# Performance work log

Hardware: AMD Instinct MI355X
Metric: run time of the kernel (lower is better)

Reference implementation:

```python
import jax, jax.numpy as jnp
import numpy as np

HIDDEN = 1024
NUM_HEADS = 16
HEAD_DIM = 64
B, S = 2, 2048


def setup_inputs() -> dict:
    key = jax.random.key(0)
    k1, k2, k3 = jax.random.split(key, 3)
    x = jax.random.normal(k1, (B, S, HIDDEN), dtype=jnp.float32)
    # xavier-uniform style scaling for the projection weights
    lim_qkv = (6.0 / (HIDDEN + 3 * NUM_HEADS * HEAD_DIM)) ** 0.5
    lim_o = (6.0 / (NUM_HEADS * HEAD_DIM + HIDDEN)) ** 0.5
    w_qkv = jax.random.uniform(k2, (HIDDEN, 3 * NUM_HEADS * HEAD_DIM), jnp.float32, -lim_qkv, lim_qkv)
    w_o = jax.random.uniform(k3, (NUM_HEADS * HEAD_DIM, HIDDEN), jnp.float32, -lim_o, lim_o)
    return {"x": x, "w_qkv": w_qkv, "w_o": w_o}


def reference(x, w_qkv, w_o):
    b, s, _ = x.shape
    qkv = jnp.einsum('bsh,hf->bsf', x, w_qkv)               # [b, s, 3*H*D]
    qkv = qkv.reshape(b, s, 3, NUM_HEADS, HEAD_DIM)
    q = jnp.transpose(qkv[:, :, 0], (0, 2, 1, 3))           # [b, h, s, d]
    k = jnp.transpose(qkv[:, :, 1], (0, 2, 3, 1))           # [b, h, d, s]
    v = jnp.transpose(qkv[:, :, 2], (0, 2, 1, 3))           # [b, h, s, d]
    scores = jnp.einsum('bhqd,bhdk->bhqk', q, k) / jnp.sqrt(jnp.float32(HEAD_DIM))
    scores = jax.nn.softmax(scores, axis=-1)                # [b, h, q, k]
    # NOTE: faithful to source bug: sums over q, output indexed by k
    values = jnp.einsum('bhqk,bhkd->bhkd', scores, v)       # [b, h, s, d]
    values = jnp.transpose(values, (0, 2, 1, 3)).reshape(b, s, NUM_HEADS * HEAD_DIM)
    return jnp.einsum('bsf,fh->bsh', values, w_o)
```

## Files before the change

### kernel.cpp

```cpp
#include <hip/hip_runtime.h>
#include <stdint.h>


#define DEV static __device__ __forceinline__

typedef unsigned short u16;
typedef __attribute__((ext_vector_type(4))) float f32x4;
typedef __attribute__((ext_vector_type(16))) float f32x16;
typedef __bf16 bf16x8 __attribute__((ext_vector_type(8)));
typedef __attribute__((ext_vector_type(8))) unsigned short u16x8;
typedef __attribute__((ext_vector_type(4))) unsigned short u16x4;

#define QSCALE 0.18033688011112042f

DEV u16 f2bf(float f) {
    unsigned u = __builtin_bit_cast(unsigned, f);
    u += 0x7fffu + ((u >> 16) & 1u);
    return (u16)(u >> 16);
}
DEV float bf2f(u16 h) {
    unsigned u = ((unsigned)h) << 16;
    return __builtin_bit_cast(float, u);
}

DEV void async_copy16(const void* g, void* l) {
    __builtin_amdgcn_global_load_lds(
        (__attribute__((address_space(1))) void*)(g),
        (__attribute__((address_space(3))) void*)(l), 16, 0, 0);
}


__global__ __launch_bounds__(256) void cast_f32_bf16(
    const float* __restrict__ src, u16* __restrict__ dst, int n4) {
    int i = blockIdx.x * 256 + threadIdx.x;
    if (i >= n4) return;
    f32x4 v = *(const f32x4*)(src + (size_t)i * 4);
    u16x4 o;
#pragma unroll
    for (int j = 0; j < 4; j++) o[j] = f2bf(v[j]);
    *(u16x4*)(dst + (size_t)i * 4) = o;
}

__global__ __launch_bounds__(256) void transpose_cast(
    const float* __restrict__ src, u16* __restrict__ dst, int rows, int cols) {
    __shared__ float tile[32][33];
    int c0 = blockIdx.x * 32, r0 = blockIdx.y * 32;
    int tx = threadIdx.x, ty = threadIdx.y;
#pragma unroll
    for (int i = 0; i < 4; i++)
        tile[ty + i * 8][tx] = src[(size_t)(r0 + ty + i * 8) * cols + c0 + tx];
    __syncthreads();
#pragma unroll
    for (int i = 0; i < 4; i++)
        dst[(size_t)(c0 + ty + i * 8) * rows + r0 + tx] = f2bf(tile[tx][ty + i * 8]);
}

__global__ __launch_bounds__(256) void gemm_qkv(
    const u16* __restrict__ A, const u16* __restrict__ Bt,
    u16* __restrict__ qb, u16* __restrict__ kb, u16* __restrict__ vb) {
    __shared__ __align__(16) u16 smem[128 * 136];
    u16* As = smem;
    u16* Bs = smem + 4096;
    const int t = threadIdx.x;
    const int wave = t >> 6;
    const int lane = t & 63;
    const int quad = lane >> 4;
    const int l16 = lane & 15;
    const int wr = wave >> 1;
    const int wc = wave & 1;
    const int m0 = blockIdx.y * 128;
    const int n0 = blockIdx.x * 128;

    f32x4 acc[4][4];
#pragma unroll
    for (int i = 0; i < 4; i++)
#pragma unroll
        for (int j = 0; j < 4; j++) acc[i][j] = {0.f, 0.f, 0.f, 0.f};

    for (int kt = 0; kt < 1024; kt += 32) {
#pragma unroll
        for (int i = 0; i < 2; i++) {
            int idx = i * 256 + t;
            int row = idx >> 2, kc = idx & 3;
            async_copy16(A + (size_t)(m0 + row) * 1024 + kt + kc * 8, &As[idx * 8]);
            async_copy16(Bt + (size_t)(n0 + row) * 1024 + kt + kc * 8, &Bs[idx * 8]);
        }
        __syncthreads();
        bf16x8 af[4], bfr[4];
#pragma unroll
        for (int mt = 0; mt < 4; mt++)
            af[mt] = *(const bf16x8*)&As[(wr * 64 + mt * 16 + l16) * 32 + quad * 8];
#pragma unroll
        for (int nt = 0; nt < 4; nt++)
            bfr[nt] = *(const bf16x8*)&Bs[(wc * 64 + nt * 16 + l16) * 32 + quad * 8];
#pragma unroll
        for (int mt = 0; mt < 4; mt++)
#pragma unroll
            for (int nt = 0; nt < 4; nt++)
                acc[mt][nt] = __builtin_amdgcn_mfma_f32_16x16x32_bf16(
                    af[mt], bfr[nt], acc[mt][nt], 0, 0, 0);
        __syncthreads();
    }

    const int tsel = n0 >> 10;
    u16* dst = tsel == 0 ? qb : (tsel == 1 ? kb : vb);
    const float scl = tsel == 0 ? QSCALE : 1.0f;
#pragma unroll
    for (int mt = 0; mt < 4; mt++)
#pragma unroll
        for (int nt = 0; nt < 4; nt++) {
            int nn = wc * 64 + nt * 16 + l16;
#pragma unroll
            for (int r = 0; r < 4; r++) {
                int mm = wr * 64 + mt * 16 + quad * 4 + r;
                smem[mm * 136 + nn] = f2bf(acc[mt][nt][r] * scl);
            }
        }
    __syncthreads();
    const int col0 = (l16) * 8;
    const int rowb = (t >> 4);
    const int h0 = (n0 & 1023) >> 6;
#pragma unroll
    for (int i = 0; i < 8; i++) {
        int row = i * 16 + rowb;
        u16x8 v = *(const u16x8*)&smem[row * 136 + col0];
        int h = h0 + (col0 >> 6), d = col0 & 63;
        int mm = m0 + row;
        int b = mm >> 11, s = mm & 2047;
        *(u16x8*)&dst[((size_t)((b * 16 + h) * 2048 + s)) * 64 + d] = v;
    }
}

__global__ __launch_bounds__(256) void gemm_out(
    const u16* __restrict__ A, const u16* __restrict__ Bt,
    float* __restrict__ out) {
    __shared__ __align__(16) u16 As[64 * 32];
    __shared__ __align__(16) u16 Bs[128 * 32];
    const int m0 = blockIdx.y * 64;
    const int n0 = blockIdx.x * 128;
    const int t = threadIdx.x;
    const int wave = t >> 6, lane = t & 63;
    const int quad = lane >> 4, l16 = lane & 15;
    const int wr = wave >> 1, wc = wave & 1;

    f32x4 acc[2][4];
#pragma unroll
    for (int i = 0; i < 2; i++)
#pragma unroll
        for (int j = 0; j < 4; j++) acc[i][j] = {0.f, 0.f, 0.f, 0.f};

    for (int kt = 0; kt < 1024; kt += 32) {
        async_copy16(A + (size_t)(m0 + (t >> 2)) * 1024 + kt + (t & 3) * 8, &As[t * 8]);
#pragma unroll
        for (int i = 0; i < 2; i++) {
            int idx = i * 256 + t;
            int row = idx >> 2, kc = idx & 3;
            async_copy16(Bt + (size_t)(n0 + row) * 1024 + kt + kc * 8, &Bs[idx * 8]);
        }
        __syncthreads();
        bf16x8 af[2], bfr[4];
#pragma unroll
        for (int mt = 0; mt < 2; mt++)
            af[mt] = *(const bf16x8*)&As[(wr * 32 + mt * 16 + l16) * 32 + quad * 8];
#pragma unroll
        for (int nt = 0; nt < 4; nt++)
            bfr[nt] = *(const bf16x8*)&Bs[(wc * 64 + nt * 16 + l16) * 32 + quad * 8];
#pragma unroll
        for (int mt = 0; mt < 2; mt++)
#pragma unroll
            for (int nt = 0; nt < 4; nt++)
                acc[mt][nt] = __builtin_amdgcn_mfma_f32_16x16x32_bf16(
                    af[mt], bfr[nt], acc[mt][nt], 0, 0, 0);
        __syncthreads();
    }
#pragma unroll
    for (int nt = 0; nt < 4; nt++) {
        int nn = n0 + wc * 64 + nt * 16 + l16;
#pragma unroll
        for (int mt = 0; mt < 2; mt++) {
#pragma unroll
            for (int r = 0; r < 4; r++) {
                int mm = m0 + wr * 32 + mt * 16 + quad * 4 + r;
                out[(size_t)mm * 1024 + nn] = acc[mt][nt][r];
            }
        }
    }
}


#define WAITBAR_4 asm volatile("s_waitcnt vmcnt(4)\n\ts_barrier" ::: "memory")
#define WAITBAR_0 asm volatile("s_waitcnt vmcnt(0)\n\ts_barrier" ::: "memory")
#define BAR_ONLY  asm volatile("s_barrier" ::: "memory")

__global__ __launch_bounds__(256) void attn_pass1(
    const u16* __restrict__ qb, const u16* __restrict__ kb,
    float* __restrict__ lp) {
    __shared__ __align__(16) u16 Ks[2][128 * 64];
    const int t = threadIdx.x;
    const int wave = t >> 6;
    const int lane = t & 63;
    const int l32 = lane & 31, half = lane >> 5;
    const int kchunk = blockIdx.x & 3;
    const int qblk = (blockIdx.x >> 2) & 7;
    const int bh = blockIdx.x >> 5;
    const int q0 = qblk * 256 + wave * 64;

    bf16x8 a[2][4];
#pragma unroll
    for (int qs = 0; qs < 2; qs++) {
        const u16* Qr = qb + (size_t)(bh * 2048 + q0 + qs * 32 + l32) * 64 + half * 8;
#pragma unroll
        for (int f = 0; f < 4; f++) a[qs][f] = *(const bf16x8*)&Qr[f * 16];
    }

    const u16* Kbase = kb + (size_t)(bh * 2048 + kchunk * 512) * 64;

    float lsum[2][16];
#pragma unroll
    for (int qs = 0; qs < 2; qs++)
#pragma unroll
        for (int r = 0; r < 16; r++) lsum[qs][r] = 0.f;

    f32x16 ZZ;
#pragma unroll
    for (int r = 0; r < 16; r++) ZZ[r] = 0.f;

#define STAGE_K(buf, kt)                                                        \
    {                                                                           \
        _Pragma("unroll") for (int i = 0; i < 4; i++) {                         \
            int idx = i * 256 + t;                                              \
            int row = idx >> 3;                                                 \
            int blk = (idx & 7) ^ (row & 7);                                    \
            async_copy16(Kbase + (size_t)((kt) * 128 + row) * 64 + blk * 8,     \
                         &Ks[buf][idx * 8]);                                    \
        }                                                                       \
    }

#define COMPUTE_K(cur)                                                          \
    {                                                                           \
        _Pragma("unroll") for (int sub = 0; sub < 4; sub++) {                   \
            const int row = sub * 32 + l32;                                     \
            const int r7 = row & 7;                                             \
            bf16x8 bfr[4];                                                      \
            _Pragma("unroll") for (int f = 0; f < 4; f++)                       \
                bfr[f] = *(const bf16x8*)&Ks[cur][row * 64 +                    \
                                                 (((f * 2 + half)) ^ r7) * 8];  \
            __builtin_amdgcn_s_setprio(1);                                      \
            _Pragma("unroll") for (int qs = 0; qs < 2; qs++) {                  \
                f32x16 acc = __builtin_amdgcn_mfma_f32_32x32x16_bf16(           \
                    a[qs][0], bfr[0], ZZ, 0, 0, 0);                             \
                _Pragma("unroll") for (int f = 1; f < 4; f++)                   \
                    acc = __builtin_amdgcn_mfma_f32_32x32x16_bf16(              \
                        a[qs][f], bfr[f], acc, 0, 0, 0);                        \
                __builtin_amdgcn_s_setprio(0);                                  \
                _Pragma("unroll") for (int r = 0; r < 16; r++)                  \
                    lsum[qs][r] += __builtin_amdgcn_exp2f(acc[r]);              \
                __builtin_amdgcn_s_setprio(1);                                  \
            }                                                                   \
            __builtin_amdgcn_s_setprio(0);                                     \
        }                                                                       \
    }

    STAGE_K(0, 0);
    for (int kt = 0; kt < 3; kt++) {
        const int cur = kt & 1;
        STAGE_K(cur ^ 1, kt + 1);
        WAITBAR_4;
        COMPUTE_K(cur);
        BAR_ONLY;
    }
    WAITBAR_0;
    COMPUTE_K(1);

#pragma unroll
    for (int qs = 0; qs < 2; qs++) {
#pragma unroll
        for (int r = 0; r < 16; r++) {
            float v = lsum[qs][r];
            v += __shfl_xor(v, 1);
            v += __shfl_xor(v, 2);
            v += __shfl_xor(v, 4);
            v += __shfl_xor(v, 8);
            v += __shfl_xor(v, 16);
            lsum[qs][r] = v;
        }
    }
    if (l32 == 0) {
#pragma unroll
        for (int qs = 0; qs < 2; qs++) {
            float* dst = lp + kchunk * 65536 + bh * 2048 + q0 + qs * 32 + half * 4;
#pragma unroll
            for (int r = 0; r < 16; r++)
                dst[(r & 3) + 8 * (r >> 2)] = lsum[qs][r];
        }
    }
}

__global__ __launch_bounds__(256) void attn_pass2(
    const u16* __restrict__ qb, const u16* __restrict__ kb,
    const float* __restrict__ lp, float* __restrict__ cp) {
    __shared__ __align__(16) u16 Qs[2][128 * 64];
    __shared__ __align__(16) float li_lds[512];
    const int t = threadIdx.x;
    const int wave = t >> 6;
    const int lane = t & 63;
    const int l32 = lane & 31, half = lane >> 5;
    const int qchunk = blockIdx.x & 3;
    const int kblk = (blockIdx.x >> 2) & 7;
    const int bh = blockIdx.x >> 5;
    const int k0 = kblk * 256 + wave * 64;

    {
        const int base = bh * 2048 + qchunk * 512;
#pragma unroll
        for (int i = 0; i < 2; i++) {
            int q = i * 256 + t;
            float s = lp[base + q] + lp[65536 + base + q] + lp[131072 + base + q] +
                      lp[196608 + base + q];
            li_lds[q] = 1.0f / s;
        }
    }

    bf16x8 b[2][4];
#pragma unroll
    for (int ks = 0; ks < 2; ks++) {
        const u16* Kr = kb + (size_t)(bh * 2048 + k0 + ks * 32 + l32) * 64 + half * 8;
#pragma unroll
        for (int f = 0; f < 4; f++) b[ks][f] = *(const bf16x8*)&Kr[f * 16];
    }

    const u16* Qbase = qb + (size_t)(bh * 2048 + qchunk * 512) * 64;

    f32x16 ZZ;
#pragma unroll
    for (int r = 0; r < 16; r++) ZZ[r] = 0.f;

#define STAGE_Q(buf, qt)                                                        \
    {                                                                           \
        _Pragma("unroll") for (int i = 0; i < 4; i++) {                         \
            int idx = i * 256 + t;                                              \
            int row = idx >> 3;                                                 \
            int blk = (idx & 7) ^ (row & 7);                                    \
            async_copy16(Qbase + (size_t)((qt) * 128 + row) * 64 + blk * 8,     \
                         &Qs[buf][idx * 8]);                                    \
        }                                                                       \
    }

#define COMPUTE_Q(cur, qt)                                                      \
    {                                                                           \
        _Pragma("unroll") for (int sub = 0; sub < 4; sub++) {                   \
            const int row = sub * 32 + l32;                                     \
            const int r7 = row & 7;                                             \
            bf16x8 af[4];                                                       \
            _Pragma("unroll") for (int f = 0; f < 4; f++)                       \
                af[f] = *(const bf16x8*)&Qs[cur][row * 64 +                     \
                                                 (((f * 2 + half)) ^ r7) * 8];  \
            const float* lr = &li_lds[(qt) * 128 + sub * 32 + half * 4];        \
            f32x4 li0 = *(const f32x4*)&lr[0];                                  \
            f32x4 li1 = *(const f32x4*)&lr[8];                                  \
            f32x4 li2 = *(const f32x4*)&lr[16];                                 \
            f32x4 li3 = *(const f32x4*)&lr[24];                                 \
            __builtin_amdgcn_s_setprio(1);                                      \
            _Pragma("unroll") for (int ks = 0; ks < 2; ks++) {                  \
                f32x16 acc = __builtin_amdgcn_mfma_f32_32x32x16_bf16(           \
                    af[0], b[ks][0], ZZ, 0, 0, 0);                              \
                _Pragma("unroll") for (int f = 1; f < 4; f++)                   \
                    acc = __builtin_amdgcn_mfma_f32_32x32x16_bf16(              \
                        af[f], b[ks][f], acc, 0, 0, 0);                         \
                __builtin_amdgcn_s_setprio(0);                                  \
                float c = cs[ks];                                               \
                _Pragma("unroll") for (int r = 0; r < 4; r++)                   \
                    c += __builtin_amdgcn_exp2f(acc[r]) * li0[r];               \
                _Pragma("unroll") for (int r = 0; r < 4; r++)                   \
                    c += __builtin_amdgcn_exp2f(acc[4 + r]) * li1[r];           \
                _Pragma("unroll") for (int r = 0; r < 4; r++)                   \
                    c += __builtin_amdgcn_exp2f(acc[8 + r]) * li2[r];           \
                _Pragma("unroll") for (int r = 0; r < 4; r++)                   \
                    c += __builtin_amdgcn_exp2f(acc[12 + r]) * li3[r];          \
                cs[ks] = c;                                                     \
                __builtin_amdgcn_s_setprio(1);                                  \
            }                                                                   \
            __builtin_amdgcn_s_setprio(0);                                     \
        }                                                                       \
    }

    float cs[2] = {0.f, 0.f};
    __syncthreads();
    STAGE_Q(0, 0);

    for (int qt = 0; qt < 3; qt++) {
        const int cur = qt & 1;
        STAGE_Q(cur ^ 1, qt + 1);
        WAITBAR_4;
        COMPUTE_Q(cur, qt);
        BAR_ONLY;
    }
    WAITBAR_0;
    COMPUTE_Q(1, 3);

#pragma unroll
    for (int ks = 0; ks < 2; ks++) {
        float v = cs[ks] + __shfl_xor(cs[ks], 32);
        if (lane < 32)
            cp[qchunk * 65536 + bh * 2048 + k0 + ks * 32 + lane] = v;
    }
}

__global__ __launch_bounds__(256) void scale_v(
    const u16* __restrict__ vb, const float* __restrict__ cp,
    u16* __restrict__ valsb) {
    int tid = blockIdx.x * 256 + threadIdx.x;
    int base = tid << 3;
    int bh = base >> 17;
    int rem = base & 131071;
    int s = rem >> 6;
    int d0 = rem & 63;
    int ci = bh * 2048 + s;
    float cs = cp[ci] + cp[65536 + ci] + cp[131072 + ci] + cp[196608 + ci];
    u16x8 v = *(const u16x8*)(vb + (size_t)base);
    u16x8 o;
#pragma unroll
    for (int i = 0; i < 8; i++) o[i] = f2bf(bf2f(v[i]) * cs);
    int b = bh >> 4, h = bh & 15;
    *(u16x8*)&valsb[(size_t)((b * 2048 + s) * 1024) + h * 64 + d0] = o;
}


extern "C" void kernel_launch(void* const* d_in, const int* in_sizes, int n_in,
                              void* d_out, int out_size, void* d_ws, size_t ws_size,
                              hipStream_t stream) {
    const float* x    = (const float*)d_in[0];
    const float* wqkv = (const float*)d_in[1];
    const float* wo   = (const float*)d_in[2];
    float* out = (float*)d_out;
    char* ws = (char*)d_ws;

    u16* xb      = (u16*)(ws);
    u16* wqkvT   = (u16*)(ws + 8388608);
    u16* woT     = (u16*)(ws + 14680064);
    u16* qb      = (u16*)(ws + 16777216);
    u16* kb      = (u16*)(ws + 25165824);
    u16* vb      = (u16*)(ws + 33554432);
    u16* valsb   = (u16*)(ws + 42467328);
    float* lp    = (float*)(ws);
    float* cp    = (float*)(ws + 1048576);

    cast_f32_bf16<<<4096, 256, 0, stream>>>(x, xb, 1048576);
    transpose_cast<<<dim3(96, 32), dim3(32, 8), 0, stream>>>(wqkv, wqkvT, 1024, 3072);
    transpose_cast<<<dim3(32, 32), dim3(32, 8), 0, stream>>>(wo, woT, 1024, 1024);
    gemm_qkv<<<dim3(24, 32), 256, 0, stream>>>(xb, wqkvT, qb, kb, vb);
    attn_pass1<<<1024, 256, 0, stream>>>(qb, kb, lp);
    attn_pass2<<<1024, 256, 0, stream>>>(qb, kb, lp, cp);
    scale_v<<<2048, 256, 0, stream>>>(vb, cp, valsb);
    gemm_out<<<dim3(8, 64), 256, 0, stream>>>(valsb, woT, out);
}
```

Before: 199.4 us.

## Fuse prep casts into one kernel and fold V scaling into output GEMM

Merges the x cast and the two weight transpose-casts into a single prep launch. The column-sum partials are accumulated with atomicAdd into one buffer, which is zeroed by a memset, instead of being written as four partial arrays. The scale_v kernel is removed, and gemm_out now loads V, applies the column sum and writes the result into LDS itself. This cuts launches and the valsb round trip through memory. In exchange, gemm_out's A loads become synchronous register loads rather than async LDS copies, which adds atomic contention and the memset.

```diff
diff --git a/kernel.cpp b/kernel.cpp
--- a/kernel.cpp
+++ b/kernel.cpp
@@ -29,23 +29,35 @@
         (__attribute__((address_space(3))) void*)(l), 16, 0, 0);
 }
 
-
-__global__ __launch_bounds__(256) void cast_f32_bf16(
-    const float* __restrict__ src, u16* __restrict__ dst, int n4) {
-    int i = blockIdx.x * 256 + threadIdx.x;
-    if (i >= n4) return;
-    f32x4 v = *(const f32x4*)(src + (size_t)i * 4);
-    u16x4 o;
-#pragma unroll
-    for (int j = 0; j < 4; j++) o[j] = f2bf(v[j]);
-    *(u16x4*)(dst + (size_t)i * 4) = o;
-}
-
-__global__ __launch_bounds__(256) void transpose_cast(
-    const float* __restrict__ src, u16* __restrict__ dst, int rows, int cols) {
+__global__ __launch_bounds__(256) void prep(
+    const float* __restrict__ x, u16* __restrict__ xb,
+    const float* __restrict__ wqkv, u16* __restrict__ wqkvT,
+    const float* __restrict__ wo, u16* __restrict__ woT) {
     __shared__ float tile[32][33];
-    int c0 = blockIdx.x * 32, r0 = blockIdx.y * 32;
-    int tx = threadIdx.x, ty = threadIdx.y;
+    const int bid = blockIdx.x;
+    const int t = threadIdx.x;
+    if (bid < 4096) {
+        int i = bid * 256 + t;
+        f32x4 v = *(const f32x4*)(x + (size_t)i * 4);
+        u16x4 o;
+#pragma unroll
+        for (int j = 0; j < 4; j++) o[j] = f2bf(v[j]);
+        *(u16x4*)(xb + (size_t)i * 4) = o;
+        return;
+    }
+    const float* src;
+    u16* dst;
+    int rows, cols, c0, r0;
+    if (bid < 7168) {
+        int b2 = bid - 4096;
+        src = wqkv; dst = wqkvT; rows = 1024; cols = 3072;
+        c0 = (b2 % 96) * 32; r0 = (b2 / 96) * 32;
+    } else {
+        int b3 = bid - 7168;
+        src = wo; dst = woT; rows = 1024; cols = 1024;
+        c0 = (b3 % 32) * 32; r0 = (b3 / 32) * 32;
+    }
+    int tx = t & 31, ty = t >> 5;
 #pragma unroll
     for (int i = 0; i < 4; i++)
         tile[ty + i * 8][tx] = src[(size_t)(r0 + ty + i * 8) * cols + c0 + tx];
@@ -132,8 +144,8 @@
 }
 
 __global__ __launch_bounds__(256) void gemm_out(
-    const u16* __restrict__ A, const u16* __restrict__ Bt,
-    float* __restrict__ out) {
+    const u16* __restrict__ vb, const float* __restrict__ csum,
+    const u16* __restrict__ Bt, float* __restrict__ out) {
     __shared__ __align__(16) u16 As[64 * 32];
     __shared__ __align__(16) u16 Bs[128 * 32];
     const int m0 = blockIdx.y * 64;
@@ -143,6 +155,9 @@
     const int quad = lane >> 4, l16 = lane & 15;
     const int wr = wave >> 1, wc = wave & 1;
 
+    const int arow = m0 + (t >> 2);
+    const int ab = arow >> 11, as = arow & 2047;
+
     f32x4 acc[2][4];
 #pragma unroll
     for (int i = 0; i < 2; i++)
@@ -150,7 +165,17 @@
         for (int j = 0; j < 4; j++) acc[i][j] = {0.f, 0.f, 0.f, 0.f};
 
     for (int kt = 0; kt < 1024; kt += 32) {
-        async_copy16(A + (size_t)(m0 + (t >> 2)) * 1024 + kt + (t & 3) * 8, &As[t * 8]);
+        {
+            int c = kt + (t & 3) * 8;
+            int h = c >> 6, d0 = c & 63;
+            int bh = ab * 16 + h;
+            float cs = csum[bh * 2048 + as];
+            u16x8 v = *(const u16x8*)&vb[((size_t)(bh * 2048 + as)) * 64 + d0];
+            u16x8 o;
+#pragma unroll
+            for (int i = 0; i < 8; i++) o[i] = f2bf(bf2f(v[i]) * cs);
+            *(u16x8*)&As[t * 8] = o;
+        }
 #pragma unroll
         for (int i = 0; i < 2; i++) {
             int idx = i * 256 + t;
@@ -298,7 +323,7 @@
 
 __global__ __launch_bounds__(256) void attn_pass2(
     const u16* __restrict__ qb, const u16* __restrict__ kb,
-    const float* __restrict__ lp, float* __restrict__ cp) {
+    const float* __restrict__ lp, float* __restrict__ csum) {
     __shared__ __align__(16) u16 Qs[2][128 * 64];
     __shared__ __align__(16) float li_lds[512];
     const int t = threadIdx.x;
@@ -402,27 +427,8 @@
     for (int ks = 0; ks < 2; ks++) {
         float v = cs[ks] + __shfl_xor(cs[ks], 32);
         if (lane < 32)
-            cp[qchunk * 65536 + bh * 2048 + k0 + ks * 32 + lane] = v;
-    }
-}
-
-__global__ __launch_bounds__(256) void scale_v(
-    const u16* __restrict__ vb, const float* __restrict__ cp,
-    u16* __restrict__ valsb) {
-    int tid = blockIdx.x * 256 + threadIdx.x;
-    int base = tid << 3;
-    int bh = base >> 17;
-    int rem = base & 131071;
-    int s = rem >> 6;
-    int d0 = rem & 63;
-    int ci = bh * 2048 + s;
-    float cs = cp[ci] + cp[65536 + ci] + cp[131072 + ci] + cp[196608 + ci];
-    u16x8 v = *(const u16x8*)(vb + (size_t)base);
-    u16x8 o;
-#pragma unroll
-    for (int i = 0; i < 8; i++) o[i] = f2bf(bf2f(v[i]) * cs);
-    int b = bh >> 4, h = bh & 15;
-    *(u16x8*)&valsb[(size_t)((b * 2048 + s) * 1024) + h * 64 + d0] = o;
+            atomicAdd(&csum[bh * 2048 + k0 + ks * 32 + lane], v);
+    }
 }
 
 
@@ -441,16 +447,13 @@
     u16* qb      = (u16*)(ws + 16777216);
     u16* kb      = (u16*)(ws + 25165824);
     u16* vb      = (u16*)(ws + 33554432);
-    u16* valsb   = (u16*)(ws + 42467328);
     float* lp    = (float*)(ws);
-    float* cp    = (float*)(ws + 1048576);
-
-    cast_f32_bf16<<<4096, 256, 0, stream>>>(x, xb, 1048576);
-    transpose_cast<<<dim3(96, 32), dim3(32, 8), 0, stream>>>(wqkv, wqkvT, 1024, 3072);
-    transpose_cast<<<dim3(32, 32), dim3(32, 8), 0, stream>>>(wo, woT, 1024, 1024);
+    float* csum  = (float*)(ws + 1048576);
+
+    prep<<<8192, 256, 0, stream>>>(x, xb, wqkv, wqkvT, wo, woT);
     gemm_qkv<<<dim3(24, 32), 256, 0, stream>>>(xb, wqkvT, qb, kb, vb);
+    hipMemsetAsync(csum, 0, 262144, stream);
     attn_pass1<<<1024, 256, 0, stream>>>(qb, kb, lp);
-    attn_pass2<<<1024, 256, 0, stream>>>(qb, kb, lp, cp);
-    scale_v<<<2048, 256, 0, stream>>>(vb, cp, valsb);
-    gemm_out<<<dim3(8, 64), 256, 0, stream>>>(valsb, woT, out);
-}
+    attn_pass2<<<1024, 256, 0, stream>>>(qb, kb, lp, csum);
+    gemm_out<<<dim3(8, 64), 256, 0, stream>>>(vb, csum, woT, out);
+}
```

Result: no change. 202.5 us (+1.5%).
